# Optimization experiments

Hardware: AMD Instinct MI355X
Metric: run time of the kernel (lower is better)

Reference implementation:

```python
import jax, jax.numpy as jnp
import numpy as np

GRID_SIZE = 5   # efficient-kan default
ORDER = 3       # spline_order default


def make_grid(in_features):
    # extended grid on [-1, 1]: (in_features, GRID_SIZE + 2*ORDER + 1)
    h = 2.0 / GRID_SIZE
    g = jnp.arange(-ORDER, GRID_SIZE + ORDER + 1, dtype=jnp.float32) * h - 1.0
    return jnp.broadcast_to(g, (in_features, g.shape[0]))


def b_splines(x, grid):
    # x: (B, I), grid: (I, G) -> (B, I, GRID_SIZE + ORDER) via Cox-de Boor
    xg = x[..., None]
    bases = ((xg >= grid[:, :-1]) & (xg < grid[:, 1:])).astype(x.dtype)
    for k in range(1, ORDER + 1):
        left = (xg - grid[:, :-(k + 1)]) / (grid[:, k:-1] - grid[:, :-(k + 1)]) * bases[..., :-1]
        right = (grid[:, k + 1:] - xg) / (grid[:, k + 1:] - grid[:, 1:-k]) * bases[..., 1:]
        bases = left + right
    return bases


def kan_linear(x, base_w, spline_w, scaler, grid):
    # base path: silu(x) @ W_b^T ; spline path: bases contracted with scaled spline weight
    bases = b_splines(x, grid)                      # (B, I, C)
    sw = spline_w * scaler[..., None]               # (O, I, C)
    return jax.nn.silu(x) @ base_w.T + jnp.einsum('bic,oic->bo', bases, sw)


def setup_inputs() -> dict:
    key = jax.random.key(0)
    ks = jax.random.split(key, 9)
    B, I, H, O, E, C = 4096, 512, 512, 512, 8, GRID_SIZE + ORDER
    s = 0.1
    return {
        'x': jax.random.normal(ks[0], (B, I), jnp.float32),
        'gate_w': jax.random.normal(ks[1], (E, I), jnp.float32) * 0.02,
        'gate_b': jnp.zeros((E,), jnp.float32),
        'base_w1': jax.random.normal(ks[2], (E, H, I), jnp.float32) * s,
        'spline_w1': jax.random.normal(ks[3], (E, H, I, C), jnp.float32) * s,
        'scaler1': jax.random.normal(ks[4], (E, H, I), jnp.float32) * s + 1.0,
        'base_w2': jax.random.normal(ks[5], (E, O, H), jnp.float32) * s,
        'spline_w2': jax.random.normal(ks[6], (E, O, H, C), jnp.float32) * s,
        'scaler2': jax.random.normal(ks[7], (E, O, H), jnp.float32) * s + 1.0,
    }


def reference(x, gate_w, gate_b, base_w1, spline_w1, scaler1, base_w2, spline_w2, scaler2):
    gate_probs = jax.nn.softmax(x @ gate_w.T + gate_b, axis=-1)  # (B, E)
    grid1 = make_grid(x.shape[-1])
    grid2 = make_grid(base_w1.shape[1])

    def expert(bw1, sw1, sc1, bw2, sw2, sc2):
        h = kan_linear(x, bw1, sw1, sc1, grid1)      # (B, H)
        return kan_linear(h, bw2, sw2, sc2, grid2)   # (B, O)

    expert_outputs = jax.vmap(expert)(base_w1, spline_w1, scaler1,
                                      base_w2, spline_w2, scaler2)  # (E, B, O)
    return jnp.einsum('be,ebo->bo', gate_probs, expert_outputs)
```

## Files before the change

kernel.cpp:

```cpp
#include <hip/hip_runtime.h>

typedef __attribute__((ext_vector_type(4))) float f32x4;
typedef __attribute__((ext_vector_type(8))) _Float16 f16x8;

#define AS1 __attribute__((address_space(1)))
#define AS3 __attribute__((address_space(3)))

__device__ __forceinline__ void async16(const void* g, void* l) {
  __builtin_amdgcn_global_load_lds((const AS1 void*)g, (AS3 void*)l, 16, 0, 0);
}

__device__ __forceinline__ void bspline8(float x, float b[8]) {
  float c[11];
#pragma unroll
  for (int j = 0; j < 11; ++j) {
    float t0 = (float)(j - 3) * 0.4f - 1.0f;
    float t1 = (float)(j - 2) * 0.4f - 1.0f;
    c[j] = (x >= t0 && x < t1) ? 1.0f : 0.0f;
  }
#pragma unroll
  for (int k = 1; k <= 3; ++k) {
#pragma unroll
    for (int j = 0; j + k < 11; ++j) {
      float tj   = (float)(j - 3) * 0.4f - 1.0f;
      float tjk  = (float)(j + k - 3) * 0.4f - 1.0f;
      float tj1  = (float)(j - 2) * 0.4f - 1.0f;
      float tjk1 = (float)(j + k - 2) * 0.4f - 1.0f;
      c[j] = (x - tj) * (1.0f / (tjk - tj)) * c[j] +
             (tjk1 - x) * (1.0f / (tjk1 - tj1)) * c[j + 1];
    }
  }
#pragma unroll
  for (int j = 0; j < 8; ++j) b[j] = c[j];
}

__global__ __launch_bounds__(256) void gate_kernel(const float* __restrict__ x,
                                                   const float* __restrict__ gw,
                                                   const float* __restrict__ gb,
                                                   float* __restrict__ gate) {
  const int b = blockIdx.x * 4 + (threadIdx.x >> 6);
  const int lane = threadIdx.x & 63;
  f32x4 x0 = *(const f32x4*)(x + ((size_t)b << 9) + lane * 8);
  f32x4 x1 = *(const f32x4*)(x + ((size_t)b << 9) + lane * 8 + 4);
  float lg[8];
#pragma unroll
  for (int e = 0; e < 8; ++e) {
    f32x4 w0 = *(const f32x4*)(gw + ((size_t)e << 9) + lane * 8);
    f32x4 w1 = *(const f32x4*)(gw + ((size_t)e << 9) + lane * 8 + 4);
    float d = 0.f;
#pragma unroll
    for (int j = 0; j < 4; ++j) d += x0[j] * w0[j] + x1[j] * w1[j];
#pragma unroll
    for (int m = 32; m >= 1; m >>= 1) d += __shfl_xor(d, m, 64);
    lg[e] = d + gb[e];
  }
  float mx = lg[0];
#pragma unroll
  for (int e = 1; e < 8; ++e) mx = fmaxf(mx, lg[e]);
  float p[8], ssum = 0.f;
#pragma unroll
  for (int e = 0; e < 8; ++e) { p[e] = __expf(lg[e] - mx); ssum += p[e]; }
  float mine = 0.f;
#pragma unroll
  for (int e = 0; e < 8; ++e) mine = (lane == e) ? p[e] / ssum : mine;
  if (lane < 8) gate[(size_t)b * 8 + lane] = mine;
}

__global__ __launch_bounds__(256) void prep_w_kernel(const float* __restrict__ bw,
                                                     const float* __restrict__ sw,
                                                     const float* __restrict__ sc,
                                                     _Float16* __restrict__ W) {
  size_t tid = (size_t)blockIdx.x * 256 + threadIdx.x;
  const size_t NSPL = (size_t)4096 * 512;
  if (tid < NSPL) {
    size_t row = tid >> 9;
    int i = (int)(tid & 511);
    float s = sc[(row << 9) + i];
    const float* sp = sw + (((row << 9) + (size_t)i) << 3);
    f32x4 v0 = *(const f32x4*)sp;
    f32x4 v1 = *(const f32x4*)(sp + 4);
    f16x8 o;
#pragma unroll
    for (int j = 0; j < 4; ++j) { o[j] = (_Float16)(v0[j] * s); o[4 + j] = (_Float16)(v1[j] * s); }
    *(f16x8*)(W + row * 4608 + 512 + (size_t)i * 8) = o;
  } else {
    size_t t2 = tid - NSPL;
    size_t row = t2 >> 6;
    int i8 = (int)((t2 & 63) << 3);
    const float* bp = bw + (row << 9) + i8;
    f32x4 v0 = *(const f32x4*)bp;
    f32x4 v1 = *(const f32x4*)(bp + 4);
    f16x8 o;
#pragma unroll
    for (int j = 0; j < 4; ++j) { o[j] = (_Float16)v0[j]; o[4 + j] = (_Float16)v1[j]; }
    *(f16x8*)(W + row * 4608 + i8) = o;
  }
}

__global__ __launch_bounds__(256) void expand_x_kernel(const float* __restrict__ x,
                                                       _Float16* __restrict__ A1, int chunk0) {
  const int tid = blockIdx.x * 256 + threadIdx.x;
  const int r = tid >> 9;
  const int i = tid & 511;
  const float xv = x[((size_t)(chunk0 + r) << 9) + i];
  const float s = xv / (1.0f + __expf(-xv));
  float bsv[8];
  bspline8(xv, bsv);
  _Float16* drow = A1 + (size_t)r * 4608;
  drow[i] = (_Float16)s;
  f16x8 v;
#pragma unroll
  for (int j = 0; j < 8; ++j) v[j] = (_Float16)bsv[j];
  *(f16x8*)(drow + 512 + (size_t)i * 8) = v;
}

template <int MODE>
__global__ __launch_bounds__(256) void kan_gemm(const _Float16* __restrict__ Abase,
                                                const _Float16* __restrict__ Wbase,
                                                _Float16* __restrict__ A2out,
                                                float* __restrict__ out_acc,
                                                const float* __restrict__ gate,
                                                int chunk0, int Mc) {
  __shared__ _Float16 As[128 * 32];
  __shared__ _Float16 Bs[128 * 32];
  const int t = threadIdx.x;
  const int z = blockIdx.z;
  const int e = (MODE == 1) ? z : (z >> 1);
  const int kbeg = (MODE == 1) ? 0 : (z & 1) * 2304;
  const int kend = (MODE == 1) ? 4608 : kbeg + 2304;
  const int tileM = blockIdx.x * 128;
  const int tileN = blockIdx.y * 128;

  const _Float16* A = (MODE == 1) ? Abase : (Abase + (size_t)e * Mc * 4608);
  const _Float16* B = Wbase + (size_t)e * 512 * 4608;

  const int srow = t >> 2;
  const int scol = (t & 3) * 8;
  const _Float16* gA0 = A + (size_t)(tileM + srow) * 4608 + scol;
  const _Float16* gA1 = A + (size_t)(tileM + 64 + srow) * 4608 + scol;
  const _Float16* gB0 = B + (size_t)(tileN + srow) * 4608 + scol;
  const _Float16* gB1 = B + (size_t)(tileN + 64 + srow) * 4608 + scol;
  _Float16* lA0 = &As[t * 8];
  _Float16* lA1 = &As[2048 + t * 8];
  _Float16* lB0 = &Bs[t * 8];
  _Float16* lB1 = &Bs[2048 + t * 8];

  const int lane = t & 63;
  const int wm = ((t >> 6) & 1) * 64;
  const int wn = ((t >> 6) >> 1) * 64;
  const int l16 = lane & 15;
  const int quad = lane >> 4;

  f32x4 acc[4][4];
#pragma unroll
  for (int i = 0; i < 4; ++i)
#pragma unroll
    for (int j = 0; j < 4; ++j) acc[i][j] = (f32x4){0.f, 0.f, 0.f, 0.f};

  for (int k0 = kbeg; k0 < kend; k0 += 32) {
    async16(gA0 + k0, lA0);
    async16(gA1 + k0, lA1);
    async16(gB0 + k0, lB0);
    async16(gB1 + k0, lB1);
    __syncthreads();
    f16x8 af[4], bfr[4];
#pragma unroll
    for (int mt = 0; mt < 4; ++mt)
      af[mt] = *(const f16x8*)(&As[(wm + mt * 16 + l16) * 32 + quad * 8]);
#pragma unroll
    for (int nt = 0; nt < 4; ++nt)
      bfr[nt] = *(const f16x8*)(&Bs[(wn + nt * 16 + l16) * 32 + quad * 8]);
#pragma unroll
    for (int mt = 0; mt < 4; ++mt)
#pragma unroll
      for (int nt = 0; nt < 4; ++nt)
        acc[mt][nt] = __builtin_amdgcn_mfma_f32_16x16x32_f16(af[mt], bfr[nt], acc[mt][nt], 0, 0, 0);
    __syncthreads();
  }

  if (MODE == 1) {
    _Float16* dst = A2out + (size_t)e * Mc * 4608;
#pragma unroll
    for (int mt = 0; mt < 4; ++mt) {
#pragma unroll
      for (int r = 0; r < 4; ++r) {
        const int m = tileM + wm + mt * 16 + quad * 4 + r;
        _Float16* drow = dst + (size_t)m * 4608;
#pragma unroll
        for (int nt = 0; nt < 4; ++nt) {
          const int n = tileN + wn + nt * 16 + l16;
          const float h = acc[mt][nt][r];
          const float s = h / (1.0f + __expf(-h));
          float bsv[8];
          bspline8(h, bsv);
          drow[n] = (_Float16)s;
          f16x8 v;
#pragma unroll
          for (int j = 0; j < 8; ++j) v[j] = (_Float16)bsv[j];
          *(f16x8*)(drow + 512 + (size_t)n * 8) = v;
        }
      }
    }
  } else {
#pragma unroll
    for (int mt = 0; mt < 4; ++mt) {
#pragma unroll
      for (int r = 0; r < 4; ++r) {
        const int m = tileM + wm + mt * 16 + quad * 4 + r;
        const float gp = gate[(size_t)(chunk0 + m) * 8 + e];
        float* orow = out_acc + (size_t)(chunk0 + m) * 512;
#pragma unroll
        for (int nt = 0; nt < 4; ++nt) {
          const int n = tileN + wn + nt * 16 + l16;
          atomicAdd(orow + n, gp * acc[mt][nt][r]);
        }
      }
    }
  }
}

extern "C" void kernel_launch(void* const* d_in, const int* in_sizes, int n_in,
                              void* d_out, int out_size, void* d_ws, size_t ws_size,
                              hipStream_t stream) {
  (void)in_sizes; (void)n_in; (void)out_size;
  const float* x   = (const float*)d_in[0];
  const float* gw  = (const float*)d_in[1];
  const float* gb  = (const float*)d_in[2];
  const float* bw1 = (const float*)d_in[3];
  const float* sw1 = (const float*)d_in[4];
  const float* sc1 = (const float*)d_in[5];
  const float* bw2 = (const float*)d_in[6];
  const float* sw2 = (const float*)d_in[7];
  const float* sc2 = (const float*)d_in[8];
  float* out = (float*)d_out;

  const size_t GATE_B = (size_t)4096 * 8 * 4;
  const size_t W_B    = (size_t)8 * 512 * 4608 * 2;
  auto al = [](size_t v) { return (v + 255) & ~(size_t)255; };

  int Mc = 128;
  const int cand[6] = {4096, 2048, 1024, 512, 256, 128};
  const size_t fixedB = al(GATE_B) + 2 * al(W_B);
  for (int ci = 0; ci < 6; ++ci) {
    size_t need = fixedB + al((size_t)cand[ci] * 4608 * 2) + al((size_t)8 * cand[ci] * 4608 * 2);
    if (need <= ws_size) { Mc = cand[ci]; break; }
  }

  char* p = (char*)d_ws;
  float* gate      = (float*)p; p += al(GATE_B);
  _Float16* W1     = (_Float16*)p; p += al(W_B);
  _Float16* W2     = (_Float16*)p; p += al(W_B);
  _Float16* A1     = (_Float16*)p; p += al((size_t)Mc * 4608 * 2);
  _Float16* A2     = (_Float16*)p;

  hipMemsetAsync(out, 0, (size_t)4096 * 512 * 4, stream);
  gate_kernel<<<1024, 256, 0, stream>>>(x, gw, gb, gate);
  prep_w_kernel<<<9216, 256, 0, stream>>>(bw1, sw1, sc1, W1);
  prep_w_kernel<<<9216, 256, 0, stream>>>(bw2, sw2, sc2, W2);

  for (int c0 = 0; c0 < 4096; c0 += Mc) {
    expand_x_kernel<<<Mc * 2, 256, 0, stream>>>(x, A1, c0);
    dim3 grid1(Mc / 128, 4, 8);
    dim3 grid2(Mc / 128, 4, 16);
    kan_gemm<1><<<grid1, 256, 0, stream>>>(A1, W1, A2, nullptr, nullptr, c0, Mc);
    kan_gemm<2><<<grid2, 256, 0, stream>>>(A2, W2, nullptr, out, gate, c0, Mc);
  }
}
```

Measured before the change: 840.9 us.

## Fuse spline expansion into second GEMM's A-tile load and drop chunking

Replaces the Cox-de Boor recursion with a closed-form uniform cubic B-spline evaluation. The first GEMM now stores only compact fp16 hidden activations h (8x4096x512), not the 9x-expanded A2 matrix. The second GEMM recomputes silu and the spline bases on the fly while filling shared memory. The aim is to cut global memory traffic and the workspace footprint, and to remove the per-chunk launch loop. In exchange, the second GEMM does more ALU work, and its A tile is filled by ordinary synchronous loads instead of async copies, with no split-K.

```diff
diff --git a/kernel.cpp b/kernel.cpp
--- a/kernel.cpp
+++ b/kernel.cpp
@@ -10,28 +10,27 @@
   __builtin_amdgcn_global_load_lds((const AS1 void*)g, (AS3 void*)l, 16, 0, 0);
 }
 
-__device__ __forceinline__ void bspline8(float x, float b[8]) {
-  float c[11];
-#pragma unroll
-  for (int j = 0; j < 11; ++j) {
-    float t0 = (float)(j - 3) * 0.4f - 1.0f;
-    float t1 = (float)(j - 2) * 0.4f - 1.0f;
-    c[j] = (x >= t0 && x < t1) ? 1.0f : 0.0f;
-  }
-#pragma unroll
-  for (int k = 1; k <= 3; ++k) {
-#pragma unroll
-    for (int j = 0; j + k < 11; ++j) {
-      float tj   = (float)(j - 3) * 0.4f - 1.0f;
-      float tjk  = (float)(j + k - 3) * 0.4f - 1.0f;
-      float tj1  = (float)(j - 2) * 0.4f - 1.0f;
-      float tjk1 = (float)(j + k - 2) * 0.4f - 1.0f;
-      c[j] = (x - tj) * (1.0f / (tjk - tj)) * c[j] +
-             (tjk1 - x) * (1.0f / (tjk1 - tj1)) * c[j + 1];
-    }
-  }
-#pragma unroll
-  for (int j = 0; j < 8; ++j) b[j] = c[j];
+__device__ __forceinline__ f16x8 expand_bases(float x) {
+  const float t0 = (float)(-3) * 0.4f - 1.0f;
+  float s = (x - t0) * 2.5f;
+  bool in = (s >= 0.0f) && (s < 11.0f);
+  int c = (int)s;
+  c = c > 10 ? 10 : c;
+  float u = s - (float)c;
+  float um = 1.0f - u;
+  float u2 = u * u, u3 = u2 * u;
+  float w3 = in ? u3 * (1.0f / 6.0f) : 0.f;
+  float w2 = in ? (1.0f + 3.0f * u + 3.0f * u2 - 3.0f * u3) * (1.0f / 6.0f) : 0.f;
+  float w1 = in ? (4.0f - 6.0f * u2 + 3.0f * u3) * (1.0f / 6.0f) : 0.f;
+  float w0 = in ? um * um * um * (1.0f / 6.0f) : 0.f;
+  f16x8 r;
+#pragma unroll
+  for (int j = 0; j < 8; ++j) {
+    int d = c - j;
+    float w = (d == 0) ? w3 : (d == 1) ? w2 : (d == 2) ? w1 : (d == 3) ? w0 : 0.f;
+    r[j] = (_Float16)w;
+  }
+  return r;
 }
 
 __global__ __launch_bounds__(256) void gate_kernel(const float* __restrict__ x,
@@ -98,46 +97,32 @@
 }
 
 __global__ __launch_bounds__(256) void expand_x_kernel(const float* __restrict__ x,
-                                                       _Float16* __restrict__ A1, int chunk0) {
+                                                       _Float16* __restrict__ A1) {
   const int tid = blockIdx.x * 256 + threadIdx.x;
   const int r = tid >> 9;
   const int i = tid & 511;
-  const float xv = x[((size_t)(chunk0 + r) << 9) + i];
+  const float xv = x[((size_t)r << 9) + i];
   const float s = xv / (1.0f + __expf(-xv));
-  float bsv[8];
-  bspline8(xv, bsv);
   _Float16* drow = A1 + (size_t)r * 4608;
   drow[i] = (_Float16)s;
-  f16x8 v;
-#pragma unroll
-  for (int j = 0; j < 8; ++j) v[j] = (_Float16)bsv[j];
-  *(f16x8*)(drow + 512 + (size_t)i * 8) = v;
-}
-
-template <int MODE>
-__global__ __launch_bounds__(256) void kan_gemm(const _Float16* __restrict__ Abase,
-                                                const _Float16* __restrict__ Wbase,
-                                                _Float16* __restrict__ A2out,
-                                                float* __restrict__ out_acc,
-                                                const float* __restrict__ gate,
-                                                int chunk0, int Mc) {
+  *(f16x8*)(drow + 512 + (size_t)i * 8) = expand_bases(xv);
+}
+
+__global__ __launch_bounds__(256) void gemm_h(const _Float16* __restrict__ A1,
+                                              const _Float16* __restrict__ W1,
+                                              _Float16* __restrict__ h) {
   __shared__ _Float16 As[128 * 32];
   __shared__ _Float16 Bs[128 * 32];
   const int t = threadIdx.x;
-  const int z = blockIdx.z;
-  const int e = (MODE == 1) ? z : (z >> 1);
-  const int kbeg = (MODE == 1) ? 0 : (z & 1) * 2304;
-  const int kend = (MODE == 1) ? 4608 : kbeg + 2304;
+  const int e = blockIdx.z;
   const int tileM = blockIdx.x * 128;
   const int tileN = blockIdx.y * 128;
-
-  const _Float16* A = (MODE == 1) ? Abase : (Abase + (size_t)e * Mc * 4608);
-  const _Float16* B = Wbase + (size_t)e * 512 * 4608;
+  const _Float16* B = W1 + (size_t)e * 512 * 4608;
 
   const int srow = t >> 2;
   const int scol = (t & 3) * 8;
-  const _Float16* gA0 = A + (size_t)(tileM + srow) * 4608 + scol;
-  const _Float16* gA1 = A + (size_t)(tileM + 64 + srow) * 4608 + scol;
+  const _Float16* gA0 = A1 + (size_t)(tileM + srow) * 4608 + scol;
+  const _Float16* gA1 = A1 + (size_t)(tileM + 64 + srow) * 4608 + scol;
   const _Float16* gB0 = B + (size_t)(tileN + srow) * 4608 + scol;
   const _Float16* gB1 = B + (size_t)(tileN + 64 + srow) * 4608 + scol;
   _Float16* lA0 = &As[t * 8];
@@ -157,7 +142,7 @@
 #pragma unroll
     for (int j = 0; j < 4; ++j) acc[i][j] = (f32x4){0.f, 0.f, 0.f, 0.f};
 
-  for (int k0 = kbeg; k0 < kend; k0 += 32) {
+  for (int k0 = 0; k0 < 4608; k0 += 32) {
     async16(gA0 + k0, lA0);
     async16(gA1 + k0, lA1);
     async16(gB0 + k0, lB0);
@@ -178,42 +163,108 @@
     __syncthreads();
   }
 
-  if (MODE == 1) {
-    _Float16* dst = A2out + (size_t)e * Mc * 4608;
-#pragma unroll
-    for (int mt = 0; mt < 4; ++mt) {
-#pragma unroll
-      for (int r = 0; r < 4; ++r) {
-        const int m = tileM + wm + mt * 16 + quad * 4 + r;
-        _Float16* drow = dst + (size_t)m * 4608;
-#pragma unroll
-        for (int nt = 0; nt < 4; ++nt) {
-          const int n = tileN + wn + nt * 16 + l16;
-          const float h = acc[mt][nt][r];
-          const float s = h / (1.0f + __expf(-h));
-          float bsv[8];
-          bspline8(h, bsv);
-          drow[n] = (_Float16)s;
-          f16x8 v;
-#pragma unroll
-          for (int j = 0; j < 8; ++j) v[j] = (_Float16)bsv[j];
-          *(f16x8*)(drow + 512 + (size_t)n * 8) = v;
-        }
+  _Float16* hd = h + (size_t)e * 4096 * 512;
+#pragma unroll
+  for (int mt = 0; mt < 4; ++mt) {
+#pragma unroll
+    for (int r = 0; r < 4; ++r) {
+      const int m = tileM + wm + mt * 16 + quad * 4 + r;
+#pragma unroll
+      for (int nt = 0; nt < 4; ++nt) {
+        const int n = tileN + wn + nt * 16 + l16;
+        hd[(size_t)m * 512 + n] = (_Float16)acc[mt][nt][r];
       }
     }
-  } else {
-#pragma unroll
-    for (int mt = 0; mt < 4; ++mt) {
-#pragma unroll
-      for (int r = 0; r < 4; ++r) {
-        const int m = tileM + wm + mt * 16 + quad * 4 + r;
-        const float gp = gate[(size_t)(chunk0 + m) * 8 + e];
-        float* orow = out_acc + (size_t)(chunk0 + m) * 512;
-#pragma unroll
-        for (int nt = 0; nt < 4; ++nt) {
-          const int n = tileN + wn + nt * 16 + l16;
-          atomicAdd(orow + n, gp * acc[mt][nt][r]);
-        }
+  }
+}
+
+__global__ __launch_bounds__(256) void gemm_out(const _Float16* __restrict__ h,
+                                                const _Float16* __restrict__ W2,
+                                                const float* __restrict__ gate,
+                                                float* __restrict__ out) {
+  __shared__ _Float16 As[128 * 32];
+  __shared__ _Float16 Bs[128 * 32];
+  const int t = threadIdx.x;
+  const int e = blockIdx.z;
+  const int tileM = blockIdx.x * 128;
+  const int tileN = blockIdx.y * 128;
+  const _Float16* hsrc = h + (size_t)e * 4096 * 512;
+  const _Float16* B = W2 + (size_t)e * 512 * 4608;
+
+  const int srow = t >> 2;
+  const int scol = (t & 3) * 8;
+  const _Float16* gB0 = B + (size_t)(tileN + srow) * 4608 + scol;
+  const _Float16* gB1 = B + (size_t)(tileN + 64 + srow) * 4608 + scol;
+  _Float16* lB0 = &Bs[t * 8];
+  _Float16* lB1 = &Bs[2048 + t * 8];
+
+  const int row = t >> 1;
+  const int half = t & 1;
+  const _Float16* hrow = hsrc + (size_t)(tileM + row) * 512;
+
+  const int lane = t & 63;
+  const int wm = ((t >> 6) & 1) * 64;
+  const int wn = ((t >> 6) >> 1) * 64;
+  const int l16 = lane & 15;
+  const int quad = lane >> 4;
+
+  f32x4 acc[4][4];
+#pragma unroll
+  for (int i = 0; i < 4; ++i)
+#pragma unroll
+    for (int j = 0; j < 4; ++j) acc[i][j] = (f32x4){0.f, 0.f, 0.f, 0.f};
+
+  for (int k0 = 0; k0 < 4608; k0 += 32) {
+    async16(gB0 + k0, lB0);
+    async16(gB1 + k0, lB1);
+    if (k0 < 512) {
+      const _Float16* hp = hrow + k0 + half * 16;
+      f16x8 h0 = *(const f16x8*)hp;
+      f16x8 h1 = *(const f16x8*)(hp + 8);
+      f16x8 s0, s1;
+#pragma unroll
+      for (int j = 0; j < 8; ++j) {
+        float v0 = (float)h0[j], v1 = (float)h1[j];
+        s0[j] = (_Float16)(v0 / (1.0f + __expf(-v0)));
+        s1[j] = (_Float16)(v1 / (1.0f + __expf(-v1)));
+      }
+      *(f16x8*)&As[row * 32 + half * 16] = s0;
+      *(f16x8*)&As[row * 32 + half * 16 + 8] = s1;
+    } else {
+      const int i0 = (k0 - 512) >> 3;
+      const int ip = half * 2;
+      const _Float16* hp = hrow + i0 + ip;
+      float ha = (float)hp[0], hb = (float)hp[1];
+      *(f16x8*)&As[row * 32 + ip * 8] = expand_bases(ha);
+      *(f16x8*)&As[row * 32 + ip * 8 + 8] = expand_bases(hb);
+    }
+    __syncthreads();
+    f16x8 af[4], bfr[4];
+#pragma unroll
+    for (int mt = 0; mt < 4; ++mt)
+      af[mt] = *(const f16x8*)(&As[(wm + mt * 16 + l16) * 32 + quad * 8]);
+#pragma unroll
+    for (int nt = 0; nt < 4; ++nt)
+      bfr[nt] = *(const f16x8*)(&Bs[(wn + nt * 16 + l16) * 32 + quad * 8]);
+#pragma unroll
+    for (int mt = 0; mt < 4; ++mt)
+#pragma unroll
+      for (int nt = 0; nt < 4; ++nt)
+        acc[mt][nt] = __builtin_amdgcn_mfma_f32_16x16x32_f16(af[mt], bfr[nt], acc[mt][nt], 0, 0, 0);
+    __syncthreads();
+  }
+
+#pragma unroll
+  for (int mt = 0; mt < 4; ++mt) {
+#pragma unroll
+    for (int r = 0; r < 4; ++r) {
+      const int m = tileM + wm + mt * 16 + quad * 4 + r;
+      const float gp = gate[(size_t)m * 8 + e];
+      float* orow = out + (size_t)m * 512;
+#pragma unroll
+      for (int nt = 0; nt < 4; ++nt) {
+        const int n = tileN + wn + nt * 16 + l16;
+        atomicAdd(orow + n, gp * acc[mt][nt][r]);
       }
     }
   }
@@ -222,7 +273,7 @@
 extern "C" void kernel_launch(void* const* d_in, const int* in_sizes, int n_in,
                               void* d_out, int out_size, void* d_ws, size_t ws_size,
                               hipStream_t stream) {
-  (void)in_sizes; (void)n_in; (void)out_size;
+  (void)in_sizes; (void)n_in; (void)out_size; (void)ws_size;
   const float* x   = (const float*)d_in[0];
   const float* gw  = (const float*)d_in[1];
   const float* gb  = (const float*)d_in[2];
@@ -234,35 +285,26 @@
   const float* sc2 = (const float*)d_in[8];
   float* out = (float*)d_out;
 
+  auto al = [](size_t v) { return (v + 255) & ~(size_t)255; };
   const size_t GATE_B = (size_t)4096 * 8 * 4;
   const size_t W_B    = (size_t)8 * 512 * 4608 * 2;
-  auto al = [](size_t v) { return (v + 255) & ~(size_t)255; };
-
-  int Mc = 128;
-  const int cand[6] = {4096, 2048, 1024, 512, 256, 128};
-  const size_t fixedB = al(GATE_B) + 2 * al(W_B);
-  for (int ci = 0; ci < 6; ++ci) {
-    size_t need = fixedB + al((size_t)cand[ci] * 4608 * 2) + al((size_t)8 * cand[ci] * 4608 * 2);
-    if (need <= ws_size) { Mc = cand[ci]; break; }
-  }
+  const size_t A1_B   = (size_t)4096 * 4608 * 2;
+  const size_t H_B    = (size_t)8 * 4096 * 512 * 2;
 
   char* p = (char*)d_ws;
-  float* gate      = (float*)p; p += al(GATE_B);
-  _Float16* W1     = (_Float16*)p; p += al(W_B);
-  _Float16* W2     = (_Float16*)p; p += al(W_B);
-  _Float16* A1     = (_Float16*)p; p += al((size_t)Mc * 4608 * 2);
-  _Float16* A2     = (_Float16*)p;
+  float* gate   = (float*)p; p += al(GATE_B);
+  _Float16* W1  = (_Float16*)p; p += al(W_B);
+  _Float16* W2  = (_Float16*)p; p += al(W_B);
+  _Float16* A1  = (_Float16*)p; p += al(A1_B);
+  _Float16* hbuf = (_Float16*)p;
 
   hipMemsetAsync(out, 0, (size_t)4096 * 512 * 4, stream);
   gate_kernel<<<1024, 256, 0, stream>>>(x, gw, gb, gate);
   prep_w_kernel<<<9216, 256, 0, stream>>>(bw1, sw1, sc1, W1);
   prep_w_kernel<<<9216, 256, 0, stream>>>(bw2, sw2, sc2, W2);
-
-  for (int c0 = 0; c0 < 4096; c0 += Mc) {
-    expand_x_kernel<<<Mc * 2, 256, 0, stream>>>(x, A1, c0);
-    dim3 grid1(Mc / 128, 4, 8);
-    dim3 grid2(Mc / 128, 4, 16);
-    kan_gemm<1><<<grid1, 256, 0, stream>>>(A1, W1, A2, nullptr, nullptr, c0, Mc);
-    kan_gemm<2><<<grid2, 256, 0, stream>>>(A2, W2, nullptr, out, gate, c0, Mc);
-  }
-}
+  expand_x_kernel<<<8192, 256, 0, stream>>>(x, A1);
+
+  dim3 grid(32, 4, 8);
+  gemm_h<<<grid, 256, 0, stream>>>(A1, W1, hbuf);
+  gemm_out<<<grid, 256, 0, stream>>>(hbuf, W2, gate, out);
+}
```

Result: slower. 1.132 ms (+34.7%).
